# Optimization experiments

Measured on AMD Instinct MI355X. Metric: run time of the kernel, lower is better.

Reference implementation:

```python
import jax, jax.numpy as jnp
import numpy as np

N, M, D = 1024, 1024, 512


def setup_inputs() -> dict:
    key = jax.random.key(0)
    ks = jax.random.split(key, 12)
    s = 1.0 / np.sqrt(D)
    return {
        "q": jax.random.normal(ks[0], (N, D), jnp.float32),
        "k": jax.random.normal(ks[1], (M, D), jnp.float32),
        "v": jax.random.normal(ks[2], (M, D), jnp.float32),
        "mask": jax.random.randint(ks[3], (N, M), 0, 2) > 0,
        "Wq": jax.random.normal(ks[4], (D, D), jnp.float32) * s,
        "bq": jax.random.normal(ks[5], (D,), jnp.float32) * s,
        "Wk": jax.random.normal(ks[6], (D, D), jnp.float32) * s,
        "bk": jax.random.normal(ks[7], (D,), jnp.float32) * s,
        "Wv": jax.random.normal(ks[8], (D, D), jnp.float32) * s,
        "bv": jax.random.normal(ks[9], (D,), jnp.float32) * s,
        "Ww": jax.random.normal(ks[10], (D,), jnp.float32) * s,
        "bw": jax.random.normal(ks[11], (1,), jnp.float32) * s,
    }


def reference(q, k, v, mask, Wq, bq, Wk, bk, Wv, bv, Ww, bw):
    # Linear projections (torch Linear: x @ W.T + b)
    qp = q @ Wq.T + bq  # [N, D]
    kp = k @ Wk.T + bk  # [M, D]
    vp = v @ Wv.T + bv  # [M, D]
    # Bahdanau additive score: W(tanh(q_n + k_m)) -> [N, M]
    h = jnp.tanh(qp[:, None, :] + kp[None, :, :])  # [N, M, D]
    scores = jnp.einsum('nmd,d->nm', h, Ww) + bw[0]
    scores = jnp.where(mask, scores, jnp.float32(-1000000.0))
    attn = jax.nn.softmax(scores, axis=1)  # softmax over M (dim 1)
    context = jnp.einsum('nm,md->nd', attn, vp)  # [N, D]
    return context
```

## Files before the change

kernel.cpp:

```cpp
#include <hip/hip_runtime.h>
#include <hip/hip_bf16.h>
#include <float.h>


#define NROWS 1024
#define DDIM  512
#define MDIM  1024

typedef __attribute__((ext_vector_type(8))) short s8v;
typedef __attribute__((ext_vector_type(4))) float f4v;
typedef __attribute__((ext_vector_type(2))) float v2f;

__device__ __forceinline__ ushort f2bf(float f) {
    unsigned u = __float_as_uint(f);
    u = u + 0x7FFFu + ((u >> 16) & 1u);
    return (ushort)(u >> 16);
}
__device__ __forceinline__ float bf2f(ushort h) {
    return __uint_as_float(((unsigned)h) << 16);
}

__device__ __forceinline__ void load_lds16(const float* g, float* l) {
    __builtin_amdgcn_global_load_lds(
        (const __attribute__((address_space(1))) void*)g,
        (__attribute__((address_space(3))) void*)l, 16, 0, 0);
}

__global__ __launch_bounds__(256) void proj_gemm(
    const float* __restrict__ q, const float* __restrict__ kk_,
    const float* __restrict__ v,
    const float* __restrict__ Wq, const float* __restrict__ bq,
    const float* __restrict__ Wk, const float* __restrict__ bk,
    const float* __restrict__ Wv, const float* __restrict__ bv,
    float* __restrict__ eq, float* __restrict__ ekT,
    ushort* __restrict__ vph, ushort* __restrict__ vpl,
    float* __restrict__ rsum, float CS)
{
    __shared__ ushort Ah[4096], Al[4096], Bh[4096], Bl[4096];

    const float* A; const float* B; const float* bias;
    int biasRow;
    if (blockIdx.z == 0)      { A = q;   B = Wq;  bias = bq; biasRow = 0; }
    else if (blockIdx.z == 1) { A = Wk;  B = kk_; bias = bk; biasRow = 1; }
    else                      { A = Wv;  B = v;   bias = bv; biasRow = 1; }

    const int bi = (blockIdx.z == 0) ? blockIdx.x : blockIdx.y;
    const int bj = (blockIdx.z == 0) ? blockIdx.y : blockIdx.x;

    const int t    = threadIdx.x;
    const int lane = t & 63;
    const int w    = t >> 6;
    const int lm   = lane & 15;
    const int lq   = lane >> 4;
    const int i0   = bi * 64;
    const int j0   = bj * 64;
    const int mh   = (w >> 1) * 32;
    const int nh   = (w & 1) * 32;

    if (blockIdx.z == 0 && bi == 0 && bj == 0) {
        float4 zz = {0.f, 0.f, 0.f, 0.f};
        *(float4*)&rsum[t * 4] = zz;
    }

    f4v acc[2][2] = {{{0.f,0.f,0.f,0.f},{0.f,0.f,0.f,0.f}},
                     {{0.f,0.f,0.f,0.f},{0.f,0.f,0.f,0.f}}};
    float4 pa[4], pb[4];

    const int sr = t >> 4, sc4 = t & 15;
#pragma unroll
    for (int p = 0; p < 4; ++p) {
        int r = sr + p * 16;
        pa[p] = *(const float4*)&A[(size_t)(i0 + r) * DDIM + sc4 * 4];
        pb[p] = *(const float4*)&B[(size_t)(j0 + r) * DDIM + sc4 * 4];
    }

    for (int kc = 0; kc < 8; ++kc) {
        __syncthreads();
#pragma unroll
        for (int p = 0; p < 4; ++p) {
            int r = sr + p * 16;
            int ad = r * 64 + (((sc4 >> 1) ^ (r & 7)) << 3) + (sc4 & 1) * 4;
            float af[4] = {pa[p].x, pa[p].y, pa[p].z, pa[p].w};
            float bf[4] = {pb[p].x, pb[p].y, pb[p].z, pb[p].w};
            ushort ah4[4], al4[4], bh4[4], bl4[4];
#pragma unroll
            for (int e = 0; e < 4; ++e) {
                ah4[e] = f2bf(af[e]); al4[e] = f2bf(af[e] - bf2f(ah4[e]));
                bh4[e] = f2bf(bf[e]); bl4[e] = f2bf(bf[e] - bf2f(bh4[e]));
            }
            *(ushort4*)&Ah[ad] = *(ushort4*)ah4;
            *(ushort4*)&Al[ad] = *(ushort4*)al4;
            *(ushort4*)&Bh[ad] = *(ushort4*)bh4;
            *(ushort4*)&Bl[ad] = *(ushort4*)bl4;
        }
        __syncthreads();
        if (kc < 7) {
            const int k0 = (kc + 1) * 64;
#pragma unroll
            for (int p = 0; p < 4; ++p) {
                int r = sr + p * 16;
                pa[p] = *(const float4*)&A[(size_t)(i0 + r) * DDIM + k0 + sc4 * 4];
                pb[p] = *(const float4*)&B[(size_t)(j0 + r) * DDIM + k0 + sc4 * 4];
            }
        }
#pragma unroll
        for (int ks = 0; ks < 2; ++ks) {
            const int kb = ks * 4 + lq;
            s8v afh[2], afl[2], bfh[2], bfl[2];
#pragma unroll
            for (int g = 0; g < 2; ++g) {
                int ra = mh + g * 16 + lm;
                int rb = nh + g * 16 + lm;
                int aa = ra * 64 + ((kb ^ (ra & 7)) << 3);
                int ab = rb * 64 + ((kb ^ (rb & 7)) << 3);
                afh[g] = *(const s8v*)&Ah[aa];
                afl[g] = *(const s8v*)&Al[aa];
                bfh[g] = *(const s8v*)&Bh[ab];
                bfl[g] = *(const s8v*)&Bl[ab];
            }
#pragma unroll
            for (int mi = 0; mi < 2; ++mi)
#pragma unroll
                for (int ni = 0; ni < 2; ++ni) {
                    acc[mi][ni] = __builtin_amdgcn_mfma_f32_16x16x32_bf16(
                        afh[mi], bfh[ni], acc[mi][ni], 0, 0, 0);
                    acc[mi][ni] = __builtin_amdgcn_mfma_f32_16x16x32_bf16(
                        afh[mi], bfl[ni], acc[mi][ni], 0, 0, 0);
                    acc[mi][ni] = __builtin_amdgcn_mfma_f32_16x16x32_bf16(
                        afl[mi], bfh[ni], acc[mi][ni], 0, 0, 0);
                }
        }
    }

    const float CLAMP = 8192.0f;
#pragma unroll
    for (int mi = 0; mi < 2; ++mi) {
#pragma unroll
        for (int ni = 0; ni < 2; ++ni) {
#pragma unroll
            for (int p = 0; p < 4; ++p) {
                int row = i0 + mh + mi * 16 + lq * 4 + p;
                int col = j0 + nh + ni * 16 + lm;
                float val = acc[mi][ni][p] + (biasRow ? bias[row] : bias[col]);
                if (blockIdx.z == 0) {
                    eq[(size_t)row * 512 + col] =
                        fminf(__builtin_amdgcn_exp2f(val * CS), CLAMP);
                } else if (blockIdx.z == 1) {
                    ekT[(size_t)row * 1024 + col] =
                        fminf(__builtin_amdgcn_exp2f(val * CS), CLAMP);
                } else {
                    ushort h = f2bf(val);
                    vph[(size_t)row * 1024 + col] = h;
                    vpl[(size_t)row * 1024 + col] = f2bf(val - bf2f(h));
                }
            }
        }
    }
}

#define DCH  32
#define SMCH 128
__global__ __launch_bounds__(256) void score_kernel(const float* __restrict__ eq,
                                                    const float* __restrict__ ekT,
                                                    const float* __restrict__ Ww,
                                                    const int* __restrict__ mask,
                                                    ushort* __restrict__ Ph,
                                                    ushort* __restrict__ Pl,
                                                    float* __restrict__ rsum)
{
    __shared__ __align__(16) float ks[DCH * SMCH];
    __shared__ __align__(16) float es[16 * DCH];
    __shared__ __align__(16) float wws[DCH];
    const int t    = threadIdx.x;
    const int lane = t & 63;
    const int w    = t >> 6;
    const int m0   = blockIdx.x * SMCH;
    const int n0   = blockIdx.y * 16;

    v2f acc[4] = {};
    const v2f one2 = {1.f, 1.f};

    for (int d0 = 0; d0 < DDIM; d0 += DCH) {
        __syncthreads();
#pragma unroll
        for (int i = 0; i < 4; ++i) {
            int r2 = w * 8 + i * 2;
            const float* g = ekT + (size_t)(d0 + r2 + (lane >> 5)) * MDIM
                             + m0 + (lane & 31) * 4;
            load_lds16(g, &ks[r2 * SMCH]);
        }
#pragma unroll
        for (int p = 0; p < 2; ++p) {
            int idx = t + p * 256;
            int nl = idx >> 5, dd = idx & 31;
            es[nl * DCH + dd] = eq[(size_t)(n0 + nl) * DDIM + d0 + dd];
        }
        if (t < DCH) wws[t] = Ww[d0 + t];
        __syncthreads();

#pragma unroll
        for (int dq = 0; dq < DCH; dq += 4) {
            v2f k0 = *(const v2f*)&ks[(dq + 0) * SMCH + lane * 2];
            v2f k1 = *(const v2f*)&ks[(dq + 1) * SMCH + lane * 2];
            v2f k2 = *(const v2f*)&ks[(dq + 2) * SMCH + lane * 2];
            v2f k3 = *(const v2f*)&ks[(dq + 3) * SMCH + lane * 2];
            float4 wg = *(const float4*)&wws[dq];
#pragma unroll
            for (int nn = 0; nn < 4; ++nn) {
                float4 eg = *(const float4*)&es[(w * 4 + nn) * DCH + dq];
                v2f A0 = __builtin_elementwise_fma(k0, (v2f){eg.x, eg.x}, one2);
                v2f A1 = __builtin_elementwise_fma(k1, (v2f){eg.y, eg.y}, one2);
                v2f A2 = __builtin_elementwise_fma(k2, (v2f){eg.z, eg.z}, one2);
                v2f A3 = __builtin_elementwise_fma(k3, (v2f){eg.w, eg.w}, one2);
                v2f n01 = __builtin_elementwise_fma((v2f){wg.y, wg.y}, A0,
                                                    (v2f){wg.x, wg.x} * A1);
                v2f d01 = A0 * A1;
                v2f n23 = __builtin_elementwise_fma((v2f){wg.w, wg.w}, A2,
                                                    (v2f){wg.z, wg.z} * A3);
                v2f d23 = A2 * A3;
                v2f num = __builtin_elementwise_fma(n01, d23, n23 * d01);
                v2f den = d01 * d23;
                v2f r = {__builtin_amdgcn_rcpf(den.x), __builtin_amdgcn_rcpf(den.y)};
                acc[nn] = __builtin_elementwise_fma(num, r, acc[nn]);
            }
        }
    }

    const float C2 = -2.8853900817779268f;
    const int m = m0 + lane * 2;
#pragma unroll
    for (int nn = 0; nn < 4; ++nn) {
        int n = n0 + w * 4 + nn;
        int2 mk = *(const int2*)&mask[(size_t)n * MDIM + m];
        float o0 = mk.x ? __builtin_amdgcn_exp2f(acc[nn].x * C2) : 0.f;
        float o1 = mk.y ? __builtin_amdgcn_exp2f(acc[nn].y * C2) : 0.f;
        ushort h0 = f2bf(o0), h1 = f2bf(o1);
        ushort l0 = f2bf(o0 - bf2f(h0)), l1 = f2bf(o1 - bf2f(h1));
        ushort2 hh = {h0, h1}, ll = {l0, l1};
        *(ushort2*)&Ph[(size_t)n * MDIM + m] = hh;
        *(ushort2*)&Pl[(size_t)n * MDIM + m] = ll;
        float rs = o0 + o1;
#pragma unroll
        for (int off = 32; off; off >>= 1) rs += __shfl_xor(rs, off);
        if (lane == 0) atomicAdd(&rsum[n], rs);
    }
}

__global__ __launch_bounds__(256) void ctx_gemm(const ushort* __restrict__ Ph,
                                                const ushort* __restrict__ Pl,
                                                const ushort* __restrict__ vph,
                                                const ushort* __restrict__ vpl,
                                                const float* __restrict__ rsum,
                                                float* __restrict__ out)
{
    const int t    = threadIdx.x;
    const int lane = t & 63;
    const int w    = t >> 6;
    const int lm   = lane & 15;
    const int lq   = lane >> 4;
    const int d0   = blockIdx.x * 64 + w * 16;
    const int n0   = blockIdx.y * 16;

    const ushort* pAh = Ph  + (size_t)(n0 + lm) * MDIM + lq * 8;
    const ushort* pAl = Pl  + (size_t)(n0 + lm) * MDIM + lq * 8;
    const ushort* pBh = vph + (size_t)(d0 + lm) * MDIM + lq * 8;
    const ushort* pBl = vpl + (size_t)(d0 + lm) * MDIM + lq * 8;

    f4v acc = {0.f, 0.f, 0.f, 0.f};
#pragma unroll 4
    for (int m0 = 0; m0 < MDIM; m0 += 32) {
        s8v ah = *(const s8v*)(pAh + m0);
        s8v al = *(const s8v*)(pAl + m0);
        s8v bh = *(const s8v*)(pBh + m0);
        s8v bl = *(const s8v*)(pBl + m0);
        acc = __builtin_amdgcn_mfma_f32_16x16x32_bf16(ah, bh, acc, 0, 0, 0);
        acc = __builtin_amdgcn_mfma_f32_16x16x32_bf16(ah, bl, acc, 0, 0, 0);
        acc = __builtin_amdgcn_mfma_f32_16x16x32_bf16(al, bh, acc, 0, 0, 0);
    }

#pragma unroll
    for (int p = 0; p < 4; ++p) {
        int nrow = n0 + lq * 4 + p;
        float inv = __builtin_amdgcn_rcpf(rsum[nrow]);
        out[(size_t)nrow * DDIM + d0 + lm] = acc[p] * inv;
    }
}

extern "C" void kernel_launch(void* const* d_in, const int* in_sizes, int n_in,
                              void* d_out, int out_size, void* d_ws, size_t ws_size,
                              hipStream_t stream)
{
    const float* q    = (const float*)d_in[0];
    const float* k    = (const float*)d_in[1];
    const float* v    = (const float*)d_in[2];
    const int*   mask = (const int*)d_in[3];
    const float* Wq   = (const float*)d_in[4];
    const float* bq   = (const float*)d_in[5];
    const float* Wk   = (const float*)d_in[6];
    const float* bk   = (const float*)d_in[7];
    const float* Wv   = (const float*)d_in[8];
    const float* bv   = (const float*)d_in[9];
    const float* Ww   = (const float*)d_in[10];

    float* ws    = (float*)d_ws;
    float* eq    = ws;
    float* ekT   = ws + 524288;
    ushort* vph  = (ushort*)(ws + 1048576);
    ushort* vpl  = (ushort*)(ws + 1310720);
    ushort* Ph   = (ushort*)(ws + 1572864);
    ushort* Pl   = (ushort*)(ws + 2097152);
    float* rsum  = ws + 2621440;
    float* out   = (float*)d_out;

    const float CS = 2.8853900817779268f;

    proj_gemm<<<dim3(16, 8, 3), dim3(256), 0, stream>>>(q, k, v, Wq, bq, Wk, bk,
                                                        Wv, bv, eq, ekT,
                                                        vph, vpl, rsum, CS);
    score_kernel<<<dim3(8, 64), dim3(256), 0, stream>>>(eq, ekT, Ww, mask,
                                                        Ph, Pl, rsum);
    ctx_gemm<<<dim3(8, 64), dim3(256), 0, stream>>>(Ph, Pl, vph, vpl, rsum, out);
}
```

Baseline: 182.9 us.

## Split ctx GEMM over M with atomics, preload score operands, use packed bf16 conversion

The context GEMM is split along M into two halves across a new grid dimension. Partial results go to the output with atomicAdd, and the projection kernel zeroes the output beforehand. The score kernel now loads the whole eq tile and Ww into LDS once, removing per-chunk global loads of those operands. Float-to-bf16 hi/lo splitting now uses the packed HIP intrinsic. Together these aim to raise parallelism and cut load/conversion overhead, at the cost of float atomics and more LDS per block, which lowers occupancy.

```diff
diff --git a/kernel.cpp b/kernel.cpp
--- a/kernel.cpp
+++ b/kernel.cpp
@@ -11,13 +11,17 @@
 typedef __attribute__((ext_vector_type(4))) float f4v;
 typedef __attribute__((ext_vector_type(2))) float v2f;
 
-__device__ __forceinline__ ushort f2bf(float f) {
-    unsigned u = __float_as_uint(f);
-    u = u + 0x7FFFu + ((u >> 16) & 1u);
-    return (ushort)(u >> 16);
-}
 __device__ __forceinline__ float bf2f(ushort h) {
     return __uint_as_float(((unsigned)h) << 16);
+}
+__device__ __forceinline__ ushort2 f2bf2(float a, float b) {
+    __hip_bfloat162 t = __float22bfloat162_rn(float2{a, b});
+    union { __hip_bfloat162 v; ushort2 u; } c; c.v = t;
+    return c.u;
+}
+__device__ __forceinline__ void hl2(float a, float b, ushort2& h, ushort2& l) {
+    h = f2bf2(a, b);
+    l = f2bf2(a - bf2f(h.x), b - bf2f(h.y));
 }
 
 __device__ __forceinline__ void load_lds16(const float* g, float* l) {
@@ -34,7 +38,7 @@
     const float* __restrict__ Wv, const float* __restrict__ bv,
     float* __restrict__ eq, float* __restrict__ ekT,
     ushort* __restrict__ vph, ushort* __restrict__ vpl,
-    float* __restrict__ rsum, float CS)
+    float* __restrict__ rsum, float* __restrict__ outz, float CS)
 {
     __shared__ ushort Ah[4096], Al[4096], Bh[4096], Bl[4096];
 
@@ -57,9 +61,14 @@
     const int mh   = (w >> 1) * 32;
     const int nh   = (w & 1) * 32;
 
-    if (blockIdx.z == 0 && bi == 0 && bj == 0) {
+    if (blockIdx.z == 0 && blockIdx.x == 0 && blockIdx.y == 0) {
+        *(float4*)&rsum[t * 4] = float4{0.f, 0.f, 0.f, 0.f};
+    } else if (blockIdx.z == 2) {
+        const int flat = blockIdx.x * 8 + blockIdx.y;
         float4 zz = {0.f, 0.f, 0.f, 0.f};
-        *(float4*)&rsum[t * 4] = zz;
+#pragma unroll
+        for (int p = 0; p < 4; ++p)
+            *(float4*)&outz[(size_t)flat * 4096 + (t + p * 256) * 4] = zz;
     }
 
     f4v acc[2][2] = {{{0.f,0.f,0.f,0.f},{0.f,0.f,0.f,0.f}},
@@ -80,18 +89,19 @@
         for (int p = 0; p < 4; ++p) {
             int r = sr + p * 16;
             int ad = r * 64 + (((sc4 >> 1) ^ (r & 7)) << 3) + (sc4 & 1) * 4;
-            float af[4] = {pa[p].x, pa[p].y, pa[p].z, pa[p].w};
-            float bf[4] = {pb[p].x, pb[p].y, pb[p].z, pb[p].w};
-            ushort ah4[4], al4[4], bh4[4], bl4[4];
-#pragma unroll
-            for (int e = 0; e < 4; ++e) {
-                ah4[e] = f2bf(af[e]); al4[e] = f2bf(af[e] - bf2f(ah4[e]));
-                bh4[e] = f2bf(bf[e]); bl4[e] = f2bf(bf[e] - bf2f(bh4[e]));
-            }
-            *(ushort4*)&Ah[ad] = *(ushort4*)ah4;
-            *(ushort4*)&Al[ad] = *(ushort4*)al4;
-            *(ushort4*)&Bh[ad] = *(ushort4*)bh4;
-            *(ushort4*)&Bl[ad] = *(ushort4*)bl4;
+            ushort2 h01, l01, h23, l23;
+            hl2(pa[p].x, pa[p].y, h01, l01);
+            hl2(pa[p].z, pa[p].w, h23, l23);
+            ushort4 ha = {h01.x, h01.y, h23.x, h23.y};
+            ushort4 la = {l01.x, l01.y, l23.x, l23.y};
+            *(ushort4*)&Ah[ad] = ha;
+            *(ushort4*)&Al[ad] = la;
+            hl2(pb[p].x, pb[p].y, h01, l01);
+            hl2(pb[p].z, pb[p].w, h23, l23);
+            ushort4 hb = {h01.x, h01.y, h23.x, h23.y};
+            ushort4 lb = {l01.x, l01.y, l23.x, l23.y};
+            *(ushort4*)&Bh[ad] = hb;
+            *(ushort4*)&Bl[ad] = lb;
         }
         __syncthreads();
         if (kc < 7) {
@@ -149,9 +159,10 @@
                     ekT[(size_t)row * 1024 + col] =
                         fminf(__builtin_amdgcn_exp2f(val * CS), CLAMP);
                 } else {
-                    ushort h = f2bf(val);
-                    vph[(size_t)row * 1024 + col] = h;
-                    vpl[(size_t)row * 1024 + col] = f2bf(val - bf2f(h));
+                    ushort2 h2 = f2bf2(val, val);
+                    vph[(size_t)row * 1024 + col] = h2.x;
+                    ushort2 l2 = f2bf2(val - bf2f(h2.x), 0.f);
+                    vpl[(size_t)row * 1024 + col] = l2.x;
                 }
             }
         }
@@ -169,14 +180,24 @@
                                                     float* __restrict__ rsum)
 {
     __shared__ __align__(16) float ks[DCH * SMCH];
-    __shared__ __align__(16) float es[16 * DCH];
-    __shared__ __align__(16) float wws[DCH];
+    __shared__ __align__(16) float es[16 * 512];
+    __shared__ __align__(16) float wws[512];
     const int t    = threadIdx.x;
     const int lane = t & 63;
     const int w    = t >> 6;
     const int m0   = blockIdx.x * SMCH;
     const int n0   = blockIdx.y * 16;
 
+#pragma unroll
+    for (int p = 0; p < 8; ++p) {
+        int idx = t + p * 256;
+        int nl = idx >> 7, dd4 = idx & 127;
+        *(float4*)&es[nl * 512 + dd4 * 4] =
+            *(const float4*)&eq[(size_t)(n0 + nl) * DDIM + dd4 * 4];
+    }
+    wws[t] = Ww[t];
+    wws[t + 256] = Ww[t + 256];
+
     v2f acc[4] = {};
     const v2f one2 = {1.f, 1.f};
 
@@ -189,13 +210,6 @@
                              + m0 + (lane & 31) * 4;
             load_lds16(g, &ks[r2 * SMCH]);
         }
-#pragma unroll
-        for (int p = 0; p < 2; ++p) {
-            int idx = t + p * 256;
-            int nl = idx >> 5, dd = idx & 31;
-            es[nl * DCH + dd] = eq[(size_t)(n0 + nl) * DDIM + d0 + dd];
-        }
-        if (t < DCH) wws[t] = Ww[d0 + t];
         __syncthreads();
 
 #pragma unroll
@@ -204,10 +218,10 @@
             v2f k1 = *(const v2f*)&ks[(dq + 1) * SMCH + lane * 2];
             v2f k2 = *(const v2f*)&ks[(dq + 2) * SMCH + lane * 2];
             v2f k3 = *(const v2f*)&ks[(dq + 3) * SMCH + lane * 2];
-            float4 wg = *(const float4*)&wws[dq];
+            float4 wg = *(const float4*)&wws[d0 + dq];
 #pragma unroll
             for (int nn = 0; nn < 4; ++nn) {
-                float4 eg = *(const float4*)&es[(w * 4 + nn) * DCH + dq];
+                float4 eg = *(const float4*)&es[(w * 4 + nn) * 512 + d0 + dq];
                 v2f A0 = __builtin_elementwise_fma(k0, (v2f){eg.x, eg.x}, one2);
                 v2f A1 = __builtin_elementwise_fma(k1, (v2f){eg.y, eg.y}, one2);
                 v2f A2 = __builtin_elementwise_fma(k2, (v2f){eg.z, eg.z}, one2);
@@ -232,14 +246,13 @@
     for (int nn = 0; nn < 4; ++nn) {
         int n = n0 + w * 4 + nn;
         int2 mk = *(const int2*)&mask[(size_t)n * MDIM + m];
-        float o0 = mk.x ? __builtin_amdgcn_exp2f(acc[nn].x * C2) : 0.f;
-        float o1 = mk.y ? __builtin_amdgcn_exp2f(acc[nn].y * C2) : 0.f;
-        ushort h0 = f2bf(o0), h1 = f2bf(o1);
-        ushort l0 = f2bf(o0 - bf2f(h0)), l1 = f2bf(o1 - bf2f(h1));
-        ushort2 hh = {h0, h1}, ll = {l0, l1};
-        *(ushort2*)&Ph[(size_t)n * MDIM + m] = hh;
-        *(ushort2*)&Pl[(size_t)n * MDIM + m] = ll;
-        float rs = o0 + o1;
+        float p0 = mk.x ? __builtin_amdgcn_exp2f(acc[nn].x * C2) : 0.f;
+        float p1 = mk.y ? __builtin_amdgcn_exp2f(acc[nn].y * C2) : 0.f;
+        ushort2 h, l;
+        hl2(p0, p1, h, l);
+        *(ushort2*)&Ph[(size_t)n * MDIM + m] = h;
+        *(ushort2*)&Pl[(size_t)n * MDIM + m] = l;
+        float rs = p0 + p1;
 #pragma unroll
         for (int off = 32; off; off >>= 1) rs += __shfl_xor(rs, off);
         if (lane == 0) atomicAdd(&rsum[n], rs);
@@ -260,15 +273,16 @@
     const int lq   = lane >> 4;
     const int d0   = blockIdx.x * 64 + w * 16;
     const int n0   = blockIdx.y * 16;
-
-    const ushort* pAh = Ph  + (size_t)(n0 + lm) * MDIM + lq * 8;
-    const ushort* pAl = Pl  + (size_t)(n0 + lm) * MDIM + lq * 8;
-    const ushort* pBh = vph + (size_t)(d0 + lm) * MDIM + lq * 8;
-    const ushort* pBl = vpl + (size_t)(d0 + lm) * MDIM + lq * 8;
+    const int mb   = blockIdx.z * 512;
+
+    const ushort* pAh = Ph  + (size_t)(n0 + lm) * MDIM + mb + lq * 8;
+    const ushort* pAl = Pl  + (size_t)(n0 + lm) * MDIM + mb + lq * 8;
+    const ushort* pBh = vph + (size_t)(d0 + lm) * MDIM + mb + lq * 8;
+    const ushort* pBl = vpl + (size_t)(d0 + lm) * MDIM + mb + lq * 8;
 
     f4v acc = {0.f, 0.f, 0.f, 0.f};
 #pragma unroll 4
-    for (int m0 = 0; m0 < MDIM; m0 += 32) {
+    for (int m0 = 0; m0 < 512; m0 += 32) {
         s8v ah = *(const s8v*)(pAh + m0);
         s8v al = *(const s8v*)(pAl + m0);
         s8v bh = *(const s8v*)(pBh + m0);
@@ -282,7 +296,7 @@
     for (int p = 0; p < 4; ++p) {
         int nrow = n0 + lq * 4 + p;
         float inv = __builtin_amdgcn_rcpf(rsum[nrow]);
-        out[(size_t)nrow * DDIM + d0 + lm] = acc[p] * inv;
+        atomicAdd(&out[(size_t)nrow * DDIM + d0 + lm], acc[p] * inv);
     }
 }
 
@@ -316,8 +330,8 @@
 
     proj_gemm<<<dim3(16, 8, 3), dim3(256), 0, stream>>>(q, k, v, Wq, bq, Wk, bk,
                                                         Wv, bv, eq, ekT,
-                                                        vph, vpl, rsum, CS);
+                                                        vph, vpl, rsum, out, CS);
     score_kernel<<<dim3(8, 64), dim3(256), 0, stream>>>(eq, ekT, Ww, mask,
                                                         Ph, Pl, rsum);
-    ctx_gemm<<<dim3(8, 64), dim3(256), 0, stream>>>(Ph, Pl, vph, vpl, rsum, out);
-}
+    ctx_gemm<<<dim3(8, 64, 2), dim3(256), 0, stream>>>(Ph, Pl, vph, vpl, rsum, out);
+}
```

New measurement: 184.7 us. Within noise of the previous version (+0.9%).
